# Kernel optimization log

Hardware: AMD Instinct MI355X
Metric: run time of the kernel (lower is better)

Reference implementation:

```python
import jax, jax.numpy as jnp
import numpy as np

# graph / model constants (match init_kwargs and input_specs)
B, NPG, EPG, ML = 4, 10000, 32000, 128      # graphs, nodes/graph, edges/graph, latent
I_LAYERS, K_ITERS, J_HEADS = 3, 4, 6         # GNN layers, outer iters (n_iter+r_iter), I*n_iter
N, E, E2 = B * NPG, B * EPG, EPG // 2
ZETA = 1e-6
P_EXP = 1.852                                # Hazen-Williams exponent


def setup_inputs() -> dict:
    rng = np.random.default_rng(0)
    sndr_l, rcvr_l, r_l = [], [], []
    for b in range(B):
        off = b * NPG
        s = rng.integers(0, NPG, E2)
        t = rng.integers(0, NPG, E2)
        # per graph: first half forward edges, second half reversed (directionality trick)
        sndr_l.append(np.concatenate([s, t]) + off)
        rcvr_l.append(np.concatenate([t, s]) + off)
        rr = rng.uniform(0.1, 1.0, (E2, 1)).astype(np.float32)
        r_l.append(np.concatenate([rr, rr], 0))
    sndr = jnp.asarray(np.concatenate(sndr_l), dtype=jnp.int32)
    rcvr = jnp.asarray(np.concatenate(rcvr_l), dtype=jnp.int32)
    r = jnp.asarray(np.concatenate(r_l, 0))
    res = rng.random(N) < 0.01
    res[np.arange(B) * NPG] = True  # at least one reservoir per graph
    h_star = np.where(res, rng.uniform(50.0, 100.0, N), 0.0).astype(np.float32)
    d_star = rng.uniform(0.0, 0.1, N).astype(np.float32)
    x = jnp.asarray(np.stack([h_star, d_star], 1))
    ks = jax.random.split(jax.random.key(0), 9)
    def w(k, shape):
        return jax.random.normal(k, shape, jnp.float32) / np.sqrt(shape[-2])
    return dict(
        x=x, r=r,
        W_node_in=w(ks[0], (2, ML)), W_edge_in=w(ks[1], (2, ML)),
        Wf1=w(ks[2], (3 * ML, ML)), Wf2=w(ks[3], (ML, ML)), Wf3=w(ks[4], (ML, 1)),
        We1=w(ks[5], (I_LAYERS, 3 * ML, ML)), We2=w(ks[6], (I_LAYERS, ML, ML)),
        Wn1=w(ks[7], (I_LAYERS, 2 * ML, ML)), Wn2=w(ks[8], (I_LAYERS, ML, ML)),
        sndr=sndr, rcvr=rcvr)


def _compute_net_flows(h, r, sndr, rcvr):
    # invert Hazen-Williams: dh = r * sign(q) * |q|^1.852  =>  q = sign(dh)*(|dh|/r)^(1/1.852)
    dh = h[sndr] - h[rcvr]
    q = jnp.sign(dh) * ((jnp.abs(dh) + ZETA) / (r + ZETA)) ** (1.0 / P_EXP)
    d = jax.ops.segment_sum(q[:, 0], rcvr, num_segments=N)[:, None]
    return d, q


def _construct_heads(h_star, q, r, sndr, rcvr):
    # physics-informed head reconstruction: propagate heads from reservoirs along edges
    res = h_star != 0
    hl = r * jnp.sign(q) * jnp.abs(q) ** P_EXP  # head loss per edge
    h = h_star
    for _ in range(J_HEADS):
        cand = (h[sndr] - hl)[:, 0]
        agg = jax.ops.segment_max(cand, rcvr, num_segments=N)[:, None]
        agg = jnp.where(agg > -1e30, agg, h)  # nodes with no incoming edge keep value
        h = jnp.where(res, h_star, jnp.maximum(h, agg))
    return h


def _forward(x, r, W_node_in, W_edge_in, Wf1, Wf2, Wf3, We1, We2, Wn1, Wn2, sndr, rcvr):
    selu = jax.nn.selu
    h_star, d_star = x[:, 0:1], x[:, 1:2]
    d_hat, q_hat = _compute_net_flows(h_star, r, sndr, rcvr)
    q_tilde = q_hat
    h_tilde = h_star
    for _ in range(K_ITERS):
        # f_1: embed node/edge features
        g = selu(jnp.concatenate([d_hat, d_star], -1)) @ W_node_in    # [N, ML]
        z = selu(jnp.concatenate([q_tilde, q_hat], -1)) @ W_edge_in   # [E, ML]
        for i in range(I_LAYERS):
            # edge update MLP on (g_sndr, g_rcvr, z), then max-aggregate to nodes
            m = selu(jnp.concatenate([g[sndr], g[rcvr], z], -1))       # [E, 3ML]
            z = selu(m @ We1[i]) @ We2[i]
            agg = jax.ops.segment_max(z, rcvr, num_segments=N)
            agg = jnp.where(agg > -1e30, agg, 0.0)
            g = selu(selu(jnp.concatenate([g, agg], -1)) @ Wn1[i]) @ Wn2[i]
        # MLP lambda: flow residual
        lam_in = selu(jnp.concatenate([g[sndr], g[rcvr], z], -1))
        q_hat = q_hat + selu(selu(lam_in @ Wf1) @ Wf2) @ Wf3
        # enforce antisymmetric directionality: q(rev) = -q(fwd)
        q_in = q_hat.reshape(B, EPG, 1)[:, :E2]
        q_hat = jnp.concatenate([q_in, -q_in], axis=1).reshape(E, 1)
        # demand reconstruction (eq. 3): scatter-add flows into receivers
        d_hat = jax.ops.segment_sum(q_hat[:, 0], rcvr, num_segments=N)[:, None]
        # f_2: physics-informed head reconstruction + net flows (eq. 6-8)
        h_tilde = _construct_heads(h_star, q_hat, r, sndr, rcvr)
        d_tilde, q_tilde = _compute_net_flows(h_tilde, r, sndr, rcvr)
    return h_tilde


def reference(x, r, W_node_in, W_edge_in, Wf1, Wf2, Wf3, We1, We2, Wn1, Wn2, sndr, rcvr):
    return _forward(x, r, W_node_in, W_edge_in, Wf1, Wf2, Wf3, We1, We2, Wn1, Wn2, sndr, rcvr)
```

## Files before the change

### kernel.cpp

```cpp
#include <hip/hip_runtime.h>
#include <hip/hip_bf16.h>
#include <math.h>

#define NPGc  10000
#define EPGc  32000
#define MLc   128
#define NNc   40000
#define NEc   128000
#define E2c   16000
#define ZETAc 1e-6f
#define INVPc 0.53995680345572354f
#define PEXPc 1.852f
#define NSB   ((NNc + 255) / 256)

typedef __attribute__((ext_vector_type(8))) short short8;
typedef __attribute__((ext_vector_type(4))) float f32x4;

__device__ __forceinline__ float selu_f(float x) {
    float e = __expf(x) - 1.0f;
    return 1.0507009873554805f * (x > 0.0f ? x : 1.6732632423543772f * e);
}
__device__ __forceinline__ void splitt(float v, unsigned& hi, unsigned& lo) {
    unsigned u = __float_as_uint(v);
    hi = u >> 16;
    float rem = v - __uint_as_float(u & 0xffff0000u);
    __hip_bfloat16 l = __float2bfloat16(rem);
    lo = (unsigned short)*reinterpret_cast<short*>(&l);
}
__device__ __forceinline__ short bf16_rne(float v) {
    __hip_bfloat16 h = __float2bfloat16(v);
    return *reinterpret_cast<short*>(&h);
}
__device__ __forceinline__ float signf(float x) {
    return (x > 0.0f) ? 1.0f : (x < 0.0f ? -1.0f : 0.0f);
}
__device__ __forceinline__ int rfl(int v) { return __builtin_amdgcn_readfirstlane(v); }

__device__ __forceinline__ void load_lds16(const void* src, void* dst) {
    __builtin_amdgcn_global_load_lds(
        (const __attribute__((address_space(1))) unsigned*)src,
        (__attribute__((address_space(3))) unsigned*)dst, 16, 0, 0);
}

#define WCA (8 * 12 * 64)
#define WCB (8 * 4 * 64)
#define WCC (8 * 8 * 64)
#define WCTOT (3 * (WCA + WCB + WCC + WCB) + WCA + WCB)

__global__ void k_wconv_all(
    const float* __restrict__ We1, const float* __restrict__ We2,
    const float* __restrict__ Wn1, const float* __restrict__ Wn2,
    const float* __restrict__ Wf1, const float* __restrict__ Wf2,
    short* __restrict__ we1h, short* __restrict__ we2h,
    short* __restrict__ wn1h, short* __restrict__ wn2h,
    short* __restrict__ wf1h, short* __restrict__ wf2h) {
    int gid = blockIdx.x * 256 + threadIdx.x;
    if (gid >= WCTOT) return;
    const float* src; short* dst; int nkc; int lg;
    if (gid < 3 * WCA) {
        int L = gid / WCA; lg = gid - L * WCA;
        src = We1 + (size_t)L * 384 * 128; dst = we1h + (size_t)L * 128 * 384; nkc = 12;
    } else if (gid < 3 * WCA + 3 * WCB) {
        int g2 = gid - 3 * WCA; int L = g2 / WCB; lg = g2 - L * WCB;
        src = We2 + (size_t)L * 128 * 128; dst = we2h + (size_t)L * 128 * 128; nkc = 4;
    } else if (gid < 3 * WCA + 3 * WCB + 3 * WCC) {
        int g2 = gid - 3 * WCA - 3 * WCB; int L = g2 / WCC; lg = g2 - L * WCC;
        src = Wn1 + (size_t)L * 256 * 128; dst = wn1h + (size_t)L * 128 * 256; nkc = 8;
    } else if (gid < 3 * WCA + 3 * WCB + 3 * WCC + 3 * WCB) {
        int g2 = gid - 3 * WCA - 3 * WCB - 3 * WCC; int L = g2 / WCB; lg = g2 - L * WCB;
        src = Wn2 + (size_t)L * 128 * 128; dst = wn2h + (size_t)L * 128 * 128; nkc = 4;
    } else if (gid < 3 * WCA + 3 * WCB + 3 * WCC + 3 * WCB + WCA) {
        lg = gid - (3 * WCA + 3 * WCB + 3 * WCC + 3 * WCB);
        src = Wf1; dst = wf1h; nkc = 12;
    } else {
        lg = gid - (3 * WCA + 3 * WCB + 3 * WCC + 3 * WCB + WCA);
        src = Wf2; dst = wf2h; nkc = 4;
    }
    int lane = lg & 63;
    int frag = lg >> 6;
    int kc = frag % nkc;
    int ct = frag / nkc;
    int col = ct * 16 + (lane & 15);
    int kbase = kc * 32 + (lane >> 4) * 8;
    size_t o = (size_t)lg * 8;
#pragma unroll
    for (int j = 0; j < 8; j++)
        dst[o + j] = bf16_rne(src[(size_t)(kbase + j) * 128 + col]);
}

__global__ void k_zero_i(int* p, int n) {
    int i = blockIdx.x * 256 + threadIdx.x;
    if (i < n) p[i] = 0;
}
__global__ void k_count(const int* __restrict__ rcvr, int* __restrict__ deg) {
    int e = blockIdx.x * 256 + threadIdx.x;
    if (e < NEc) atomicAdd(&deg[rcvr[e]], 1);
}
__global__ void k_scan1(const int* __restrict__ deg, int* __restrict__ partial) {
    __shared__ int buf[256];
    int t = threadIdx.x;
    int i = blockIdx.x * 256 + t;
    buf[t] = (i < NNc) ? deg[i] : 0;
    __syncthreads();
    for (int off = 128; off > 0; off >>= 1) {
        if (t < off) buf[t] += buf[t + off];
        __syncthreads();
    }
    if (t == 0) partial[blockIdx.x] = buf[0];
}
__global__ void k_scan2(int* __restrict__ partial) {
    __shared__ int buf[256];
    int t = threadIdx.x;
    int v = (t < NSB) ? partial[t] : 0;
    buf[t] = v;
    __syncthreads();
    for (int off = 1; off < 256; off <<= 1) {
        int u = (t >= off) ? buf[t - off] : 0;
        __syncthreads();
        buf[t] += u;
        __syncthreads();
    }
    if (t < NSB) partial[t] = buf[t] - v;
}
__global__ void k_scan3(const int* __restrict__ deg, const int* __restrict__ partial,
                        int* __restrict__ rowstart, int* __restrict__ cursor) {
    __shared__ int buf[256];
    int t = threadIdx.x;
    int i = blockIdx.x * 256 + t;
    int v = (i < NNc) ? deg[i] : 0;
    buf[t] = v;
    __syncthreads();
    for (int off = 1; off < 256; off <<= 1) {
        int u = (t >= off) ? buf[t - off] : 0;
        __syncthreads();
        buf[t] += u;
        __syncthreads();
    }
    int excl = partial[blockIdx.x] + buf[t] - v;
    if (i < NNc) { rowstart[i] = excl; cursor[i] = excl; }
    if (i == NNc - 1) rowstart[NNc] = excl + v;
}
__global__ void k_scatter(const int* __restrict__ sndr, const int* __restrict__ rcvr,
                          int* __restrict__ cursor, int2* __restrict__ csr_se) {
    int e = blockIdx.x * 256 + threadIdx.x;
    if (e >= NEc) return;
    int rv = rcvr[e];
    int p = atomicAdd(&cursor[rv], 1);
    csr_se[p] = make_int2(sndr[e], e);
}

__global__ void k_qinit(const float* __restrict__ x, const float* __restrict__ r,
                        const int* __restrict__ sndr, const int* __restrict__ rcvr,
                        float* __restrict__ qh, float* __restrict__ qt) {
    int e = blockIdx.x * 256 + threadIdx.x;
    if (e >= NEc) return;
    float hv = x[2 * sndr[e]] - x[2 * rcvr[e]];
    float q = signf(hv) * __powf((fabsf(hv) + ZETAc) / (r[e] + ZETAc), INVPc);
    qh[e] = q; qt[e] = q;
}
__global__ void k_flows_q(const float* __restrict__ h, const float* __restrict__ r,
                          const int* __restrict__ sndr, const int* __restrict__ rcvr,
                          float* __restrict__ qt) {
    int e = blockIdx.x * 256 + threadIdx.x;
    if (e >= NEc) return;
    float hv = h[sndr[e]] - h[rcvr[e]];
    qt[e] = signf(hv) * __powf((fabsf(hv) + ZETAc) / (r[e] + ZETAc), INVPc);
}

__global__ __launch_bounds__(256) void k_node_in_f(
    const float* __restrict__ qh, const int* __restrict__ rowstart,
    const int2* __restrict__ csr_se, const float* __restrict__ x,
    const float* __restrict__ W ,
    unsigned* __restrict__ gh_u, unsigned* __restrict__ gl_u) {
    const int tid = threadIdx.x;
    const int lane = tid & 63;
    const int n = rfl(blockIdx.x * 4 + (tid >> 6));
    if (n >= NNc) return;
    int p0 = rfl(rowstart[n]), p1 = rfl(rowstart[n + 1]);
    float s = 0.0f;
    for (int p = p0 + lane; p < p1; p += 64) s += qh[csr_se[p].y];
#pragma unroll
    for (int off = 1; off < 64; off <<= 1) s += __shfl_xor(s, off, 64);
    float s0 = selu_f(s);
    float s1 = selu_f(x[2 * n + 1]);
    int c = lane * 2;
    float g0 = s0 * W[c]     + s1 * W[MLc + c];
    float g1 = s0 * W[c + 1] + s1 * W[MLc + c + 1];
    unsigned h0, l0, h1, l1;
    splitt(selu_f(g0), h0, l0);
    splitt(selu_f(g1), h1, l1);
    gh_u[(size_t)n * 64 + lane] = h0 | (h1 << 16);
    gl_u[(size_t)n * 64 + lane] = l0 | (l1 << 16);
}

__global__ __launch_bounds__(256) void k_head_iter(
    const float* __restrict__ x, const float* __restrict__ hin, int hstride,
    const float* __restrict__ hl, const int* __restrict__ rowstart,
    const int2* __restrict__ csr_se, float* __restrict__ hout) {
    int t = blockIdx.x * 256 + threadIdx.x;
    int n = t >> 2;
    int sub = t & 3;
    if (n >= NNc) return;
    float hv = hin[(size_t)n * hstride];
    float m = -3.0e38f;
    int p0 = rowstart[n], p1 = rowstart[n + 1];
    for (int p = p0 + sub; p < p1; p += 4) {
        int2 se = csr_se[p];
        m = fmaxf(m, hin[(size_t)se.x * hstride] - hl[se.y]);
    }
    m = fmaxf(m, __shfl_xor(m, 1, 64));
    m = fmaxf(m, __shfl_xor(m, 2, 64));
    if (sub == 0) {
        float a = (m > -1e30f) ? m : hv;
        float hstar = x[2 * n];
        hout[n] = (hstar != 0.0f) ? hstar : fmaxf(hv, a);
    }
}


__global__ __launch_bounds__(512) void k_edge_mlp_mfma(
    const unsigned* __restrict__ gh_u, const unsigned* __restrict__ gl_u,
    const unsigned* __restrict__ zh_u, const unsigned* __restrict__ zl_u,
    short* __restrict__ zoh_s, short* __restrict__ zol_s,
    const short* __restrict__ W1h, const short* __restrict__ W2h,
    const int* __restrict__ sndr, const int* __restrict__ rcvr,
    const float* __restrict__ qt, const float* __restrict__ qh,
    const float* __restrict__ Wei, int zmode) {
    __shared__ short smem[24576];
    const int tid = threadIdx.x;
    const int bi = blockIdx.x;
    const int x7 = bi & 7, jj = bi >> 3;
    const int e0 = ((x7 >> 1) * 1000 + (x7 & 1) * 500 + jj) * 32;
    const int lane = tid & 63, wave = tid >> 6;
    const int l15 = lane & 15, quad = lane >> 4;

    {
        const int plane = wave & 1;
        const int rt = (wave >> 1) & 1;
        const int kc0 = wave >> 2;
        const int erow = e0 + rt * 16 + l15;
        const size_t bs = (size_t)sndr[erow] * 64 + quad * 4;
        const size_t br = (size_t)rcvr[erow] * 64 + quad * 4;
        const size_t bz = (size_t)erow * 64 + quad * 4;
        const unsigned* pg = plane ? gl_u : gh_u;
        const unsigned* pz = plane ? zl_u : zh_u;
        short* dbase = smem + plane * 12288 + rt * 512;
        const int nkc = zmode ? 8 : 12;
#pragma unroll
        for (int u = 0; u < 6; u++) {
            int kc = kc0 + 2 * u;
            if (kc < nkc) {
                int region = kc >> 2, kcl = kc & 3;
                const unsigned* src =
                    (region == 0) ? (pg + bs + kcl * 16)
                  : (region == 1) ? (pg + br + kcl * 16)
                                  : (pz + bz + kcl * 16);
                load_lds16(src, dbase + kc * 1024);
            }
        }
        if (zmode) {
            const int kcz = wave >> 1;
            const int rtz = wave & 1;
            const int e = e0 + rtz * 16 + l15;
            const float sqt = selu_f(qt[e]), sqh = selu_f(qh[e]);
            short8 vh, vl;
#pragma unroll
            for (int j = 0; j < 8; j++) {
                int c = kcz * 32 + quad * 8 + j;
                float z = sqt * Wei[c] + sqh * Wei[MLc + c];
                unsigned h, l;
                splitt(selu_f(z), h, l);
                vh[j] = (short)h; vl[j] = (short)l;
            }
            int fr = (8 + kcz) * 2 + rtz;
            *(short8*)&smem[fr * 512 + lane * 8] = vh;
            *(short8*)&smem[12288 + fr * 512 + lane * 8] = vl;
        }
    }
    __syncthreads();

    const int ct = wave;
    const int col = ct * 16 + l15;
    const short* abase = smem + lane * 8;

    f32x4 acc[2];
    acc[0] = (f32x4){0.f, 0.f, 0.f, 0.f};
    acc[1] = (f32x4){0.f, 0.f, 0.f, 0.f};
#pragma unroll
    for (int kc = 0; kc < 12; kc++) {
        size_t wo = ((size_t)(ct * 12 + kc) * 64 + lane) * 8;
        short8 bh = *(const short8*)&W1h[wo];
#pragma unroll
        for (int rt = 0; rt < 2; rt++) {
            const short* ap = abase + (kc * 2 + rt) * 512;
            short8 ah = *(const short8*)ap;
            short8 al = *(const short8*)(ap + 12288);
            acc[rt] = __builtin_amdgcn_mfma_f32_16x16x32_bf16(ah, bh, acc[rt], 0, 0, 0);
            acc[rt] = __builtin_amdgcn_mfma_f32_16x16x32_bf16(al, bh, acc[rt], 0, 0, 0);
        }
    }
    __syncthreads();
    {
        const int kc2 = ct >> 1;
        const int q2 = ((ct & 1) << 1) | (l15 >> 3);
        const int jj2 = l15 & 7;
#pragma unroll
        for (int rt = 0; rt < 2; rt++) {
#pragma unroll
            for (int rr = 0; rr < 4; rr++) {
                unsigned h, l;
                splitt(selu_f(acc[rt][rr]), h, l);
                int o = (kc2 * 2 + rt) * 512 + (q2 * 16 + quad * 4 + rr) * 8 + jj2;
                smem[o] = (short)h;
                smem[4096 + o] = (short)l;
            }
        }
    }
    __syncthreads();

    f32x4 acc2[2];
    acc2[0] = (f32x4){0.f, 0.f, 0.f, 0.f};
    acc2[1] = (f32x4){0.f, 0.f, 0.f, 0.f};
#pragma unroll
    for (int kc = 0; kc < 4; kc++) {
        size_t wo = ((size_t)(ct * 4 + kc) * 64 + lane) * 8;
        short8 bh = *(const short8*)&W2h[wo];
#pragma unroll
        for (int rt = 0; rt < 2; rt++) {
            const short* ap = abase + (kc * 2 + rt) * 512;
            short8 ah = *(const short8*)ap;
            short8 al = *(const short8*)(ap + 4096);
            acc2[rt] = __builtin_amdgcn_mfma_f32_16x16x32_bf16(ah, bh, acc2[rt], 0, 0, 0);
            acc2[rt] = __builtin_amdgcn_mfma_f32_16x16x32_bf16(al, bh, acc2[rt], 0, 0, 0);
        }
    }
#pragma unroll
    for (int rt = 0; rt < 2; rt++) {
#pragma unroll
        for (int rr = 0; rr < 4; rr++) {
            unsigned h, l;
            splitt(selu_f(acc2[rt][rr]), h, l);
            size_t o = (size_t)(e0 + rt * 16 + quad * 4 + rr) * 128 + col;
            zoh_s[o] = (short)h;
            zol_s[o] = (short)l;
        }
    }
}

__global__ __launch_bounds__(512) void k_node_mlp_mfma(
    const unsigned* __restrict__ gh_u, const unsigned* __restrict__ gl_u,
    short* __restrict__ goh_s, short* __restrict__ gol_s,
    const unsigned* __restrict__ zh_u, const unsigned* __restrict__ zl_u,
    const int* __restrict__ rowstart, const int2* __restrict__ csr_se,
    const short* __restrict__ W1h, const short* __restrict__ W2h) {
    __shared__ short smem[16384];
    const int tid = threadIdx.x;
    const int n0 = blockIdx.x * 32;
    const int lane = tid & 63, wave = tid >> 6;
    const int l15 = lane & 15, quad = lane >> 4;

    {
        const int plane = wave & 1;
        const int rt = (wave >> 1) & 1;
        const int kc0 = wave >> 2;
        const size_t bg = (size_t)(n0 + rt * 16 + l15) * 64 + quad * 4;
        const unsigned* pg = plane ? gl_u : gh_u;
        short* dbase = smem + plane * 8192 + rt * 512;
#pragma unroll
        for (int u = 0; u < 2; u++) {
            int kc = kc0 + 2 * u;
            load_lds16(pg + bg + kc * 16, dbase + kc * 1024);
        }
    }
    for (int idx = tid; idx < 32 * 64; idx += 512) {
        int row = rfl(idx >> 6);
        int cp = idx & 63;
        int n = rfl(n0 + row);
        int p0 = rfl(rowstart[n]), p1 = rfl(rowstart[n + 1]);
        float b0 = -3.0e38f, b1 = -3.0e38f;
        unsigned bh0 = 0, bl0 = 0, bh1 = 0, bl1 = 0;
        for (int p = p0; p < p1; p++) {
            int ey = rfl(csr_se[p].y);
            size_t o = (size_t)ey * 64 + cp;
            unsigned vh = zh_u[o], vl = zl_u[o];
            float f0 = __uint_as_float(vh << 16) + __uint_as_float(vl << 16);
            float f1 = __uint_as_float(vh & 0xffff0000u) + __uint_as_float(vl & 0xffff0000u);
            if (f0 > b0) { b0 = f0; bh0 = vh & 0xffffu; bl0 = vl & 0xffffu; }
            if (f1 > b1) { b1 = f1; bh1 = vh & 0xffff0000u; bl1 = vl & 0xffff0000u; }
        }
        int rt = row >> 4;
        int kc = 4 + (cp >> 4);
        int o2 = (kc * 2 + rt) * 512 + (((cp >> 2) & 3) * 16 + (row & 15)) * 8 + 2 * (cp & 3);
        *(unsigned*)&smem[o2] = bh0 | bh1;
        *(unsigned*)&smem[8192 + o2] = bl0 | bl1;
    }
    __syncthreads();

    const int ct = wave;
    const int col = ct * 16 + l15;
    const short* abase = smem + lane * 8;

    f32x4 acc[2];
    acc[0] = (f32x4){0.f, 0.f, 0.f, 0.f};
    acc[1] = (f32x4){0.f, 0.f, 0.f, 0.f};
#pragma unroll
    for (int kc = 0; kc < 8; kc++) {
        size_t wo = ((size_t)(ct * 8 + kc) * 64 + lane) * 8;
        short8 bh = *(const short8*)&W1h[wo];
#pragma unroll
        for (int rt = 0; rt < 2; rt++) {
            const short* ap = abase + (kc * 2 + rt) * 512;
            short8 ah = *(const short8*)ap;
            short8 al = *(const short8*)(ap + 8192);
            acc[rt] = __builtin_amdgcn_mfma_f32_16x16x32_bf16(ah, bh, acc[rt], 0, 0, 0);
            acc[rt] = __builtin_amdgcn_mfma_f32_16x16x32_bf16(al, bh, acc[rt], 0, 0, 0);
        }
    }
    __syncthreads();
    {
        const int kc2 = ct >> 1;
        const int q2 = ((ct & 1) << 1) | (l15 >> 3);
        const int jj2 = l15 & 7;
#pragma unroll
        for (int rt = 0; rt < 2; rt++) {
#pragma unroll
            for (int rr = 0; rr < 4; rr++) {
                unsigned h, l;
                splitt(selu_f(acc[rt][rr]), h, l);
                int o = (kc2 * 2 + rt) * 512 + (q2 * 16 + quad * 4 + rr) * 8 + jj2;
                smem[o] = (short)h;
                smem[4096 + o] = (short)l;
            }
        }
    }
    __syncthreads();

    f32x4 acc2[2];
    acc2[0] = (f32x4){0.f, 0.f, 0.f, 0.f};
    acc2[1] = (f32x4){0.f, 0.f, 0.f, 0.f};
#pragma unroll
    for (int kc = 0; kc < 4; kc++) {
        size_t wo = ((size_t)(ct * 4 + kc) * 64 + lane) * 8;
        short8 bh = *(const short8*)&W2h[wo];
#pragma unroll
        for (int rt = 0; rt < 2; rt++) {
            const short* ap = abase + (kc * 2 + rt) * 512;
            short8 ah = *(const short8*)ap;
            short8 al = *(const short8*)(ap + 4096);
            acc2[rt] = __builtin_amdgcn_mfma_f32_16x16x32_bf16(ah, bh, acc2[rt], 0, 0, 0);
            acc2[rt] = __builtin_amdgcn_mfma_f32_16x16x32_bf16(al, bh, acc2[rt], 0, 0, 0);
        }
    }
#pragma unroll
    for (int rt = 0; rt < 2; rt++) {
#pragma unroll
        for (int rr = 0; rr < 4; rr++) {
            unsigned h, l;
            splitt(selu_f(acc2[rt][rr]), h, l);
            size_t o = (size_t)(n0 + rt * 16 + quad * 4 + rr) * 128 + col;
            goh_s[o] = (short)h;
            gol_s[o] = (short)l;
        }
    }
}

__global__ __launch_bounds__(512) void k_wf_mfma(
    const unsigned* __restrict__ gh_u, const unsigned* __restrict__ gl_u,
    const unsigned* __restrict__ zh_u, const unsigned* __restrict__ zl_u,
    const short* __restrict__ W1h, const short* __restrict__ W2h,
    const float* __restrict__ W3 ,
    const int* __restrict__ sndr, const int* __restrict__ rcvr,
    const float* __restrict__ r,
    float* __restrict__ qh, float* __restrict__ hl) {
    __shared__ short smem[24576];
    __shared__ float red[32 * 8];
    const int tid = threadIdx.x;
    const int bi = blockIdx.x;
    const int x7 = bi & 7, jj = bi >> 3;
    const int fi0 = ((x7 >> 1) * 500 + (x7 & 1) * 250 + jj) * 32;
    const int b = fi0 / E2c;
    const int ebase = b * EPGc - b * E2c;
    const int lane = tid & 63, wave = tid >> 6;
    const int l15 = lane & 15, quad = lane >> 4;

    {
        const int plane = wave & 1;
        const int rt = (wave >> 1) & 1;
        const int kc0 = wave >> 2;
        const int erow = ebase + fi0 + rt * 16 + l15;
        const size_t bs = (size_t)sndr[erow] * 64 + quad * 4;
        const size_t br = (size_t)rcvr[erow] * 64 + quad * 4;
        const size_t bz = (size_t)erow * 64 + quad * 4;
        const unsigned* pg = plane ? gl_u : gh_u;
        const unsigned* pz = plane ? zl_u : zh_u;
        short* dbase = smem + plane * 12288 + rt * 512;
#pragma unroll
        for (int u = 0; u < 6; u++) {
            int kc = kc0 + 2 * u;
            int region = kc >> 2, kcl = kc & 3;
            const unsigned* src =
                (region == 0) ? (pg + bs + kcl * 16)
              : (region == 1) ? (pg + br + kcl * 16)
                              : (pz + bz + kcl * 16);
            load_lds16(src, dbase + kc * 1024);
        }
    }
    __syncthreads();

    const int ct = wave;
    const int col = ct * 16 + l15;
    const short* abase = smem + lane * 8;

    f32x4 acc[2];
    acc[0] = (f32x4){0.f, 0.f, 0.f, 0.f};
    acc[1] = (f32x4){0.f, 0.f, 0.f, 0.f};
#pragma unroll
    for (int kc = 0; kc < 12; kc++) {
        size_t wo = ((size_t)(ct * 12 + kc) * 64 + lane) * 8;
        short8 bh = *(const short8*)&W1h[wo];
#pragma unroll
        for (int rt = 0; rt < 2; rt++) {
            const short* ap = abase + (kc * 2 + rt) * 512;
            short8 ah = *(const short8*)ap;
            short8 al = *(const short8*)(ap + 12288);
            acc[rt] = __builtin_amdgcn_mfma_f32_16x16x32_bf16(ah, bh, acc[rt], 0, 0, 0);
            acc[rt] = __builtin_amdgcn_mfma_f32_16x16x32_bf16(al, bh, acc[rt], 0, 0, 0);
        }
    }
    __syncthreads();
    {
        const int kc2 = ct >> 1;
        const int q2 = ((ct & 1) << 1) | (l15 >> 3);
        const int jj2 = l15 & 7;
#pragma unroll
        for (int rt = 0; rt < 2; rt++) {
#pragma unroll
            for (int rr = 0; rr < 4; rr++) {
                unsigned h, l;
                splitt(selu_f(acc[rt][rr]), h, l);
                int o = (kc2 * 2 + rt) * 512 + (q2 * 16 + quad * 4 + rr) * 8 + jj2;
                smem[o] = (short)h;
                smem[4096 + o] = (short)l;
            }
        }
    }
    __syncthreads();

    f32x4 acc2[2];
    acc2[0] = (f32x4){0.f, 0.f, 0.f, 0.f};
    acc2[1] = (f32x4){0.f, 0.f, 0.f, 0.f};
#pragma unroll
    for (int kc = 0; kc < 4; kc++) {
        size_t wo = ((size_t)(ct * 4 + kc) * 64 + lane) * 8;
        short8 bh = *(const short8*)&W2h[wo];
#pragma unroll
        for (int rt = 0; rt < 2; rt++) {
            const short* ap = abase + (kc * 2 + rt) * 512;
            short8 ah = *(const short8*)ap;
            short8 al = *(const short8*)(ap + 4096);
            acc2[rt] = __builtin_amdgcn_mfma_f32_16x16x32_bf16(ah, bh, acc2[rt], 0, 0, 0);
            acc2[rt] = __builtin_amdgcn_mfma_f32_16x16x32_bf16(al, bh, acc2[rt], 0, 0, 0);
        }
    }
    float w3 = W3[col];
    float p[8];
#pragma unroll
    for (int rt = 0; rt < 2; rt++)
#pragma unroll
        for (int rr = 0; rr < 4; rr++) p[rt * 4 + rr] = selu_f(acc2[rt][rr]) * w3;
#pragma unroll
    for (int off = 1; off < 16; off <<= 1) {
#pragma unroll
        for (int i = 0; i < 8; i++) p[i] += __shfl_xor(p[i], off, 64);
    }
    if (l15 == 0) {
#pragma unroll
        for (int rt = 0; rt < 2; rt++)
#pragma unroll
            for (int rr = 0; rr < 4; rr++)
                red[(rt * 16 + quad * 4 + rr) * 8 + ct] = p[rt * 4 + rr];
    }
    __syncthreads();
    if (tid < 32) {
        float f = 0.0f;
#pragma unroll
        for (int c = 0; c < 8; c++) f += red[tid * 8 + c];
        int e = ebase + fi0 + tid;
        float qn = qh[e] + f;
        qh[e] = qn;
        qh[e + E2c] = -qn;
        float hv = r[e] * signf(qn) * __powf(fabsf(qn), PEXPc);
        hl[e] = hv;
        hl[e + E2c] = -hv;
    }
}


extern "C" void kernel_launch(void* const* d_in, const int* in_sizes, int n_in,
                              void* d_out, int out_size, void* d_ws, size_t ws_size,
                              hipStream_t stream) {
    const float* x   = (const float*)d_in[0];
    const float* r   = (const float*)d_in[1];
    const float* Wni = (const float*)d_in[2];
    const float* Wei = (const float*)d_in[3];
    const float* Wf1 = (const float*)d_in[4];
    const float* Wf2 = (const float*)d_in[5];
    const float* Wf3 = (const float*)d_in[6];
    const float* We1 = (const float*)d_in[7];
    const float* We2 = (const float*)d_in[8];
    const float* Wn1 = (const float*)d_in[9];
    const float* Wn2 = (const float*)d_in[10];
    const int* sndr  = (const int*)d_in[11];
    const int* rcvr  = (const int*)d_in[12];
    float* out = (float*)d_out;

    char* wp = (char*)d_ws;
    auto carve = [&](size_t bytes) -> void* {
        void* ret = (void*)wp;
        wp += (bytes + 255) & ~(size_t)255;
        return ret;
    };
    unsigned* gh_u = (unsigned*)carve((size_t)NNc * 64 * 4);
    unsigned* gl_u = (unsigned*)carve((size_t)NNc * 64 * 4);
    unsigned* zAh  = (unsigned*)carve((size_t)NEc * 64 * 4);
    unsigned* zAl  = (unsigned*)carve((size_t)NEc * 64 * 4);
    unsigned* zBh  = (unsigned*)carve((size_t)NEc * 64 * 4);
    unsigned* zBl  = (unsigned*)carve((size_t)NEc * 64 * 4);
    float* qh     = (float*)carve((size_t)NEc * 4);
    float* qt     = (float*)carve((size_t)NEc * 4);
    float* hl     = (float*)carve((size_t)NEc * 4);
    float* hA     = (float*)carve((size_t)NNc * 4);
    float* hB     = (float*)carve((size_t)NNc * 4);
    int*   deg    = (int*)carve((size_t)NNc * 4);
    int*   cursor = (int*)carve((size_t)NNc * 4);
    int*   rowst  = (int*)carve((size_t)(NNc + 1) * 4);
    int*   part   = (int*)carve((size_t)NSB * 4);
    int2*  csr_se = (int2*)carve((size_t)NEc * 8);
    short* we1h   = (short*)carve((size_t)3 * 128 * 384 * 2);
    short* we2h   = (short*)carve((size_t)3 * 128 * 128 * 2);
    short* wn1h   = (short*)carve((size_t)3 * 128 * 256 * 2);
    short* wn2h   = (short*)carve((size_t)3 * 128 * 128 * 2);
    short* wf1h   = (short*)carve((size_t)128 * 384 * 2);
    short* wf2h   = (short*)carve((size_t)128 * 128 * 2);

    const int TB = 256;
    const int gN  = (NNc + TB - 1) / TB;
    const int gE  = (NEc + TB - 1) / TB;

    k_wconv_all<<<(WCTOT + TB - 1) / TB, TB, 0, stream>>>(
        We1, We2, Wn1, Wn2, Wf1, Wf2, we1h, we2h, wn1h, wn2h, wf1h, wf2h);

    k_zero_i<<<gN, TB, 0, stream>>>(deg, NNc);
    k_count<<<gE, TB, 0, stream>>>(rcvr, deg);
    k_scan1<<<NSB, TB, 0, stream>>>(deg, part);
    k_scan2<<<1, TB, 0, stream>>>(part);
    k_scan3<<<NSB, TB, 0, stream>>>(deg, part, rowst, cursor);
    k_scatter<<<gE, TB, 0, stream>>>(sndr, rcvr, cursor, csr_se);

    k_qinit<<<gE, TB, 0, stream>>>(x, r, sndr, rcvr, qh, qt);

    const int gH = (NNc * 4 + 255) / 256;
    for (int kit = 0; kit < 4; kit++) {
        k_node_in_f<<<(NNc + 3) / 4, TB, 0, stream>>>(qh, rowst, csr_se, x, Wni, gh_u, gl_u);
        unsigned *zin_h = zAh, *zin_l = zAl, *zout_h = zAh, *zout_l = zAl;
        for (int i = 0; i < 3; i++) {
            zin_h = zout_h; zin_l = zout_l;
            zout_h = (i & 1) ? zAh : zBh;
            zout_l = (i & 1) ? zAl : zBl;
            k_edge_mlp_mfma<<<NEc / 32, 512, 0, stream>>>(
                gh_u, gl_u, zin_h, zin_l, (short*)zout_h, (short*)zout_l,
                we1h + (size_t)i * 128 * 384,
                we2h + (size_t)i * 128 * 128,
                sndr, rcvr, qt, qh, Wei, (i == 0) ? 1 : 0);
            k_node_mlp_mfma<<<NNc / 32, 512, 0, stream>>>(
                gh_u, gl_u, (short*)gh_u, (short*)gl_u, zout_h, zout_l, rowst, csr_se,
                wn1h + (size_t)i * 128 * 256,
                wn2h + (size_t)i * 128 * 128);
        }
        k_wf_mfma<<<(4 * E2c) / 32, 512, 0, stream>>>(
            gh_u, gl_u, zout_h, zout_l, wf1h, wf2h, Wf3, sndr, rcvr,
            r, qh, hl);
        const float* hin = x; int hstride = 2;
        float* cur = hA;
        for (int jh = 0; jh < 6; jh++) {
            float* dst = (jh == 5) ? ((kit == 3) ? out : hB) : cur;
            k_head_iter<<<gH, TB, 0, stream>>>(x, hin, hstride, hl, rowst, csr_se, dst);
            hin = dst; hstride = 1;
            cur = (dst == hA) ? hB : hA;
        }
        if (kit < 3) k_flows_q<<<gE, TB, 0, stream>>>(hB, r, sndr, rcvr, qt);
    }
}
```

Measured before the change: 1.441 ms.

## Halve edge-MLP LDS footprint by staging K in two halves, add setprio around MFMA

The edge MLP and lambda MLP kernels now load the 384-wide gathered input into LDS in two 6-chunk halves instead of all at once. This halves shared memory per block so more blocks can be resident per CU. The cost is an extra pair of barriers and a second gather phase that is serialized behind the first half's MFMA work. s_setprio raises wave priority around the MFMA loops in all three MLP kernels so other waves' memory traffic can overlap with them.

```diff
diff --git a/kernel.cpp b/kernel.cpp
--- a/kernel.cpp
+++ b/kernel.cpp
@@ -226,7 +226,7 @@
     const int* __restrict__ sndr, const int* __restrict__ rcvr,
     const float* __restrict__ qt, const float* __restrict__ qh,
     const float* __restrict__ Wei, int zmode) {
-    __shared__ short smem[24576];
+    __shared__ short smem[12288];
     const int tid = threadIdx.x;
     const int bi = blockIdx.x;
     const int x7 = bi & 7, jj = bi >> 3;
@@ -234,48 +234,40 @@
     const int lane = tid & 63, wave = tid >> 6;
     const int l15 = lane & 15, quad = lane >> 4;
 
-    {
-        const int plane = wave & 1;
-        const int rt = (wave >> 1) & 1;
-        const int kc0 = wave >> 2;
-        const int erow = e0 + rt * 16 + l15;
-        const size_t bs = (size_t)sndr[erow] * 64 + quad * 4;
-        const size_t br = (size_t)rcvr[erow] * 64 + quad * 4;
-        const size_t bz = (size_t)erow * 64 + quad * 4;
-        const unsigned* pg = plane ? gl_u : gh_u;
-        const unsigned* pz = plane ? zl_u : zh_u;
-        short* dbase = smem + plane * 12288 + rt * 512;
-        const int nkc = zmode ? 8 : 12;
-#pragma unroll
-        for (int u = 0; u < 6; u++) {
-            int kc = kc0 + 2 * u;
-            if (kc < nkc) {
-                int region = kc >> 2, kcl = kc & 3;
-                const unsigned* src =
-                    (region == 0) ? (pg + bs + kcl * 16)
-                  : (region == 1) ? (pg + br + kcl * 16)
-                                  : (pz + bz + kcl * 16);
-                load_lds16(src, dbase + kc * 1024);
-            }
-        }
-        if (zmode) {
-            const int kcz = wave >> 1;
-            const int rtz = wave & 1;
-            const int e = e0 + rtz * 16 + l15;
-            const float sqt = selu_f(qt[e]), sqh = selu_f(qh[e]);
-            short8 vh, vl;
-#pragma unroll
-            for (int j = 0; j < 8; j++) {
-                int c = kcz * 32 + quad * 8 + j;
-                float z = sqt * Wei[c] + sqh * Wei[MLc + c];
-                unsigned h, l;
-                splitt(selu_f(z), h, l);
-                vh[j] = (short)h; vl[j] = (short)l;
-            }
-            int fr = (8 + kcz) * 2 + rtz;
-            *(short8*)&smem[fr * 512 + lane * 8] = vh;
-            *(short8*)&smem[12288 + fr * 512 + lane * 8] = vl;
-        }
+    const int plane = wave & 1;
+    const int srt = (wave >> 1) & 1;
+    const int kc0 = wave >> 2;
+    const int erow = e0 + srt * 16 + l15;
+    const size_t bs = (size_t)sndr[erow] * 64 + quad * 4;
+    const size_t br = (size_t)rcvr[erow] * 64 + quad * 4;
+    const size_t bz = (size_t)erow * 64 + quad * 4;
+    const unsigned* pg = plane ? gl_u : gh_u;
+    const unsigned* pz = plane ? zl_u : zh_u;
+    short* dbase = smem + plane * 6144 + srt * 512;
+    const int nkc = zmode ? 8 : 12;
+
+    short8 zvh, zvl;
+    const int kzi = wave >> 1, rtz = wave & 1;
+    if (zmode) {
+        const int e = e0 + rtz * 16 + l15;
+        const float sqt = selu_f(qt[e]), sqh = selu_f(qh[e]);
+#pragma unroll
+        for (int j = 0; j < 8; j++) {
+            int c = kzi * 32 + quad * 8 + j;
+            float z = sqt * Wei[c] + sqh * Wei[MLc + c];
+            unsigned h, l;
+            splitt(selu_f(z), h, l);
+            zvh[j] = (short)h; zvl[j] = (short)l;
+        }
+    }
+
+#pragma unroll
+    for (int u = 0; u < 3; u++) {
+        int kc = kc0 + 2 * u;
+        int region = kc >> 2, kcl = kc & 3;
+        const unsigned* src = (region == 0) ? (pg + bs + kcl * 16)
+                                            : (pg + br + kcl * 16);
+        load_lds16(src, dbase + kc * 1024);
     }
     __syncthreads();
 
@@ -286,20 +278,58 @@
     f32x4 acc[2];
     acc[0] = (f32x4){0.f, 0.f, 0.f, 0.f};
     acc[1] = (f32x4){0.f, 0.f, 0.f, 0.f};
-#pragma unroll
-    for (int kc = 0; kc < 12; kc++) {
+    __builtin_amdgcn_s_setprio(1);
+#pragma unroll
+    for (int kc = 0; kc < 6; kc++) {
         size_t wo = ((size_t)(ct * 12 + kc) * 64 + lane) * 8;
         short8 bh = *(const short8*)&W1h[wo];
 #pragma unroll
         for (int rt = 0; rt < 2; rt++) {
             const short* ap = abase + (kc * 2 + rt) * 512;
             short8 ah = *(const short8*)ap;
-            short8 al = *(const short8*)(ap + 12288);
+            short8 al = *(const short8*)(ap + 6144);
             acc[rt] = __builtin_amdgcn_mfma_f32_16x16x32_bf16(ah, bh, acc[rt], 0, 0, 0);
             acc[rt] = __builtin_amdgcn_mfma_f32_16x16x32_bf16(al, bh, acc[rt], 0, 0, 0);
         }
     }
-    __syncthreads();
+    __builtin_amdgcn_s_setprio(0);
+    __syncthreads();
+
+#pragma unroll
+    for (int u = 0; u < 3; u++) {
+        int kc = 6 + kc0 + 2 * u;
+        if (kc < nkc) {
+            int region = kc >> 2, kcl = kc & 3;
+            const unsigned* src = (region == 1) ? (pg + br + kcl * 16)
+                                                : (pz + bz + kcl * 16);
+            load_lds16(src, dbase + (kc - 6) * 1024);
+        }
+    }
+    if (zmode) {
+        int slot = (2 + kzi) * 2 + rtz;
+        *(short8*)&smem[slot * 512 + lane * 8] = zvh;
+        *(short8*)&smem[6144 + slot * 512 + lane * 8] = zvl;
+    }
+    __syncthreads();
+
+    __builtin_amdgcn_s_setprio(1);
+#pragma unroll
+    for (int kc6 = 0; kc6 < 6; kc6++) {
+        int kc = 6 + kc6;
+        size_t wo = ((size_t)(ct * 12 + kc) * 64 + lane) * 8;
+        short8 bh = *(const short8*)&W1h[wo];
+#pragma unroll
+        for (int rt = 0; rt < 2; rt++) {
+            const short* ap = abase + (kc6 * 2 + rt) * 512;
+            short8 ah = *(const short8*)ap;
+            short8 al = *(const short8*)(ap + 6144);
+            acc[rt] = __builtin_amdgcn_mfma_f32_16x16x32_bf16(ah, bh, acc[rt], 0, 0, 0);
+            acc[rt] = __builtin_amdgcn_mfma_f32_16x16x32_bf16(al, bh, acc[rt], 0, 0, 0);
+        }
+    }
+    __builtin_amdgcn_s_setprio(0);
+    __syncthreads();
+
     {
         const int kc2 = ct >> 1;
         const int q2 = ((ct & 1) << 1) | (l15 >> 3);
@@ -321,6 +351,7 @@
     f32x4 acc2[2];
     acc2[0] = (f32x4){0.f, 0.f, 0.f, 0.f};
     acc2[1] = (f32x4){0.f, 0.f, 0.f, 0.f};
+    __builtin_amdgcn_s_setprio(1);
 #pragma unroll
     for (int kc = 0; kc < 4; kc++) {
         size_t wo = ((size_t)(ct * 4 + kc) * 64 + lane) * 8;
@@ -334,6 +365,7 @@
             acc2[rt] = __builtin_amdgcn_mfma_f32_16x16x32_bf16(al, bh, acc2[rt], 0, 0, 0);
         }
     }
+    __builtin_amdgcn_s_setprio(0);
 #pragma unroll
     for (int rt = 0; rt < 2; rt++) {
 #pragma unroll
@@ -403,6 +435,7 @@
     f32x4 acc[2];
     acc[0] = (f32x4){0.f, 0.f, 0.f, 0.f};
     acc[1] = (f32x4){0.f, 0.f, 0.f, 0.f};
+    __builtin_amdgcn_s_setprio(1);
 #pragma unroll
     for (int kc = 0; kc < 8; kc++) {
         size_t wo = ((size_t)(ct * 8 + kc) * 64 + lane) * 8;
@@ -416,6 +449,7 @@
             acc[rt] = __builtin_amdgcn_mfma_f32_16x16x32_bf16(al, bh, acc[rt], 0, 0, 0);
         }
     }
+    __builtin_amdgcn_s_setprio(0);
     __syncthreads();
     {
         const int kc2 = ct >> 1;
@@ -438,6 +472,7 @@
     f32x4 acc2[2];
     acc2[0] = (f32x4){0.f, 0.f, 0.f, 0.f};
     acc2[1] = (f32x4){0.f, 0.f, 0.f, 0.f};
+    __builtin_amdgcn_s_setprio(1);
 #pragma unroll
     for (int kc = 0; kc < 4; kc++) {
         size_t wo = ((size_t)(ct * 4 + kc) * 64 + lane) * 8;
@@ -451,6 +486,7 @@
             acc2[rt] = __builtin_amdgcn_mfma_f32_16x16x32_bf16(al, bh, acc2[rt], 0, 0, 0);
         }
     }
+    __builtin_amdgcn_s_setprio(0);
 #pragma unroll
     for (int rt = 0; rt < 2; rt++) {
 #pragma unroll
@@ -472,7 +508,7 @@
     const int* __restrict__ sndr, const int* __restrict__ rcvr,
     const float* __restrict__ r,
     float* __restrict__ qh, float* __restrict__ hl) {
-    __shared__ short smem[24576];
+    __shared__ short smem[12288];
     __shared__ float red[32 * 8];
     const int tid = threadIdx.x;
     const int bi = blockIdx.x;
@@ -483,27 +519,24 @@
     const int lane = tid & 63, wave = tid >> 6;
     const int l15 = lane & 15, quad = lane >> 4;
 
-    {
-        const int plane = wave & 1;
-        const int rt = (wave >> 1) & 1;
-        const int kc0 = wave >> 2;
-        const int erow = ebase + fi0 + rt * 16 + l15;
-        const size_t bs = (size_t)sndr[erow] * 64 + quad * 4;
-        const size_t br = (size_t)rcvr[erow] * 64 + quad * 4;
-        const size_t bz = (size_t)erow * 64 + quad * 4;
-        const unsigned* pg = plane ? gl_u : gh_u;
-        const unsigned* pz = plane ? zl_u : zh_u;
-        short* dbase = smem + plane * 12288 + rt * 512;
-#pragma unroll
-        for (int u = 0; u < 6; u++) {
-            int kc = kc0 + 2 * u;
-            int region = kc >> 2, kcl = kc & 3;
-            const unsigned* src =
-                (region == 0) ? (pg + bs + kcl * 16)
-              : (region == 1) ? (pg + br + kcl * 16)
-                              : (pz + bz + kcl * 16);
-            load_lds16(src, dbase + kc * 1024);
-        }
+    const int plane = wave & 1;
+    const int srt = (wave >> 1) & 1;
+    const int kc0 = wave >> 2;
+    const int erow = ebase + fi0 + srt * 16 + l15;
+    const size_t bs = (size_t)sndr[erow] * 64 + quad * 4;
+    const size_t br = (size_t)rcvr[erow] * 64 + quad * 4;
+    const size_t bz = (size_t)erow * 64 + quad * 4;
+    const unsigned* pg = plane ? gl_u : gh_u;
+    const unsigned* pz = plane ? zl_u : zh_u;
+    short* dbase = smem + plane * 6144 + srt * 512;
+
+#pragma unroll
+    for (int u = 0; u < 3; u++) {
+        int kc = kc0 + 2 * u;
+        int region = kc >> 2, kcl = kc & 3;
+        const unsigned* src = (region == 0) ? (pg + bs + kcl * 16)
+                                            : (pg + br + kcl * 16);
+        load_lds16(src, dbase + kc * 1024);
     }
     __syncthreads();
 
@@ -514,20 +547,51 @@
     f32x4 acc[2];
     acc[0] = (f32x4){0.f, 0.f, 0.f, 0.f};
     acc[1] = (f32x4){0.f, 0.f, 0.f, 0.f};
-#pragma unroll
-    for (int kc = 0; kc < 12; kc++) {
+    __builtin_amdgcn_s_setprio(1);
+#pragma unroll
+    for (int kc = 0; kc < 6; kc++) {
         size_t wo = ((size_t)(ct * 12 + kc) * 64 + lane) * 8;
         short8 bh = *(const short8*)&W1h[wo];
 #pragma unroll
         for (int rt = 0; rt < 2; rt++) {
             const short* ap = abase + (kc * 2 + rt) * 512;
             short8 ah = *(const short8*)ap;
-            short8 al = *(const short8*)(ap + 12288);
+            short8 al = *(const short8*)(ap + 6144);
             acc[rt] = __builtin_amdgcn_mfma_f32_16x16x32_bf16(ah, bh, acc[rt], 0, 0, 0);
             acc[rt] = __builtin_amdgcn_mfma_f32_16x16x32_bf16(al, bh, acc[rt], 0, 0, 0);
         }
     }
-    __syncthreads();
+    __builtin_amdgcn_s_setprio(0);
+    __syncthreads();
+
+#pragma unroll
+    for (int u = 0; u < 3; u++) {
+        int kc = 6 + kc0 + 2 * u;
+        int region = kc >> 2, kcl = kc & 3;
+        const unsigned* src = (region == 1) ? (pg + br + kcl * 16)
+                                            : (pz + bz + kcl * 16);
+        load_lds16(src, dbase + (kc - 6) * 1024);
+    }
+    __syncthreads();
+
+    __builtin_amdgcn_s_setprio(1);
+#pragma unroll
+    for (int kc6 = 0; kc6 < 6; kc6++) {
+        int kc = 6 + kc6;
+        size_t wo = ((size_t)(ct * 12 + kc) * 64 + lane) * 8;
+        short8 bh = *(const short8*)&W1h[wo];
+#pragma unroll
+        for (int rt = 0; rt < 2; rt++) {
+            const short* ap = abase + (kc6 * 2 + rt) * 512;
+            short8 ah = *(const short8*)ap;
+            short8 al = *(const short8*)(ap + 6144);
+            acc[rt] = __builtin_amdgcn_mfma_f32_16x16x32_bf16(ah, bh, acc[rt], 0, 0, 0);
+            acc[rt] = __builtin_amdgcn_mfma_f32_16x16x32_bf16(al, bh, acc[rt], 0, 0, 0);
+        }
+    }
+    __builtin_amdgcn_s_setprio(0);
+    __syncthreads();
+
     {
         const int kc2 = ct >> 1;
         const int q2 = ((ct & 1) << 1) | (l15 >> 3);
@@ -549,6 +613,7 @@
     f32x4 acc2[2];
     acc2[0] = (f32x4){0.f, 0.f, 0.f, 0.f};
     acc2[1] = (f32x4){0.f, 0.f, 0.f, 0.f};
+    __builtin_amdgcn_s_setprio(1);
 #pragma unroll
     for (int kc = 0; kc < 4; kc++) {
         size_t wo = ((size_t)(ct * 4 + kc) * 64 + lane) * 8;
@@ -562,6 +627,7 @@
             acc2[rt] = __builtin_amdgcn_mfma_f32_16x16x32_bf16(al, bh, acc2[rt], 0, 0, 0);
         }
     }
+    __builtin_amdgcn_s_setprio(0);
     float w3 = W3[col];
     float p[8];
 #pragma unroll
```

Result: faster. 1.389 ms, median of 3 (-3.6%).
